# Performance work log

Hardware: AMD Instinct MI355X
Metric: run time of the kernel (lower is better)

The kernel has to match this reference:

```python
import jax, jax.numpy as jnp
import numpy as np

EPS = 1e-5

def _causal_conv(x, w):
    # x: [B, Cin, S], w: [Cout, Cin, K]; left-pad by K-1 for causality
    k = w.shape[-1]
    x = jnp.pad(x, ((0, 0), (0, 0), (k - 1, 0)))
    return jax.lax.conv_general_dilated(x, w, (1,), 'VALID',
                                        dimension_numbers=('NCH', 'OIH', 'NCH'))

def _activate_norm(x):
    # relu -> mean-center over last axis -> scaled L2 normalize over last axis
    x = jax.nn.relu(x)
    x = x - x.mean(-1, keepdims=True)
    n = x.shape[-1]
    denom = (jnp.sqrt(jnp.sum(x * x, axis=-1, keepdims=True)) + EPS) * (n ** -0.5)
    return x / denom

def _feed_forward(x, w0, w1, w2):
    x = _causal_conv(x, w0)
    x = _activate_norm(x)
    x = _causal_conv(x, w1)
    x = _activate_norm(x)
    return _causal_conv(x, w2)

def setup_inputs() -> dict:
    key = jax.random.key(0)
    B, F, S = 4, 1024, 2048
    I, K = 2048, 5
    ks = jax.random.split(key, 12)
    def w(k, shape):
        fan_in = shape[1] * shape[2]
        return jax.random.normal(k, shape, jnp.float32) * (fan_in ** -0.5)
    inp = jax.random.normal(ks[0], (B, F, S), jnp.float32)
    pos_embd = jax.random.normal(ks[1], (1, F, S), jnp.float32) * 0.02
    divisor = jax.random.uniform(ks[2], (1, F, S), jnp.float32) + 0.5  # bounded away from 0
    return {
        'inp': inp, 'pos_embd': pos_embd, 'divisor': divisor,
        'dw0': w(ks[3], (I, F, 1)), 'dw1': w(ks[4], (I, I, K)), 'dw2': w(ks[5], (F, I, 1)),
        'sw0': w(ks[6], (I, F, 1)), 'sw1': w(ks[7], (I, I, K)), 'sw2': w(ks[8], (F, I, 1)),
        'hw0': w(ks[9], (I, F, 1)), 'hw1': w(ks[10], (I, I, K)), 'hw2': w(ks[11], (F, I, 1)),
    }

def reference(inp, pos_embd, divisor, dw0, dw1, dw2, sw0, sw1, sw2, hw0, hw1, hw2):
    out = inp + pos_embd
    depth = _feed_forward(out, dw0, dw1, dw2)
    scale = _feed_forward(out, sw0, sw1, sw2)
    shift = _feed_forward(out, hw0, hw1, hw2)
    # linear attention: cumsum over dim 1 (as in source), divide, scale/shift, norm, residual
    return inp + _activate_norm(jnp.cumsum(depth, axis=1) / divisor * scale + shift)
```

## Files before the change

### kernel.cpp

```cpp
#include <hip/hip_runtime.h>
#include <math.h>

#define BSZ 4
#define FCH 1024
#define SEQ 2048
#define ICH 2048
#define KW  5
#define EPSV 1e-5f
#define RPAD 2244
#define NCHF 16

typedef __attribute__((ext_vector_type(8))) short bf16x8;
typedef __attribute__((ext_vector_type(4))) float f32x4;
typedef __attribute__((ext_vector_type(4))) unsigned short us4;

__device__ __forceinline__ unsigned short f2bf(float f) {
  union { float f; unsigned u; } v; v.f = f;
  unsigned r = v.u + 0x7fff + ((v.u >> 16) & 1);
  return (unsigned short)(r >> 16);
}
__device__ __forceinline__ float bf2f(unsigned short u) {
  union { unsigned u; float f; } v; v.u = (unsigned)u << 16; return v.f;
}

__device__ __forceinline__ void gload_lds16(const void* g, void* l) {
  __builtin_amdgcn_global_load_lds(
      (const __attribute__((address_space(1))) void*)g,
      (__attribute__((address_space(3))) void*)l, 16, 0, 0);
}

__global__ __launch_bounds__(256) void addpos_T_kernel(
    const float* __restrict__ inp, const float* __restrict__ pos,
    unsigned short* __restrict__ X)
{
  __shared__ float t[64][65];
  const int s0 = blockIdx.x * 64, f0 = blockIdx.y * 64, b = blockIdx.z;
  const int a = threadIdx.x & 63, g = threadIdx.x >> 6;
  const float* ib = inp + (size_t)b * FCH * SEQ;
#pragma unroll
  for (int i = 0; i < 16; ++i) {
    const size_t o = (size_t)(f0 + g + i * 4) * SEQ + s0 + a;
    t[a][g + i * 4] = ib[o] + pos[o];
  }
  __syncthreads();
#pragma unroll
  for (int i = 0; i < 16; ++i)
    X[(size_t)b * RPAD * FCH + (size_t)(4 + s0 + g + i * 4) * FCH + f0 + a] =
        f2bf(t[g + i * 4][a]);
}

__global__ __launch_bounds__(256) void zero_xpad_kernel(unsigned short* __restrict__ X)
{
  const int i = blockIdx.x * 256 + threadIdx.x;
  const int b = i / (4 * FCH);
  const int r = i % (4 * FCH);
  X[(size_t)b * RPAD * FCH + r] = 0;
}

__global__ __launch_bounds__(256) void transpose_div_kernel(
    const float* __restrict__ D, float* __restrict__ O)
{
  __shared__ float t[64][65];
  const int s0 = blockIdx.x * 64, f0 = blockIdx.y * 64;
  const int a = threadIdx.x & 63, g = threadIdx.x >> 6;
#pragma unroll
  for (int i = 0; i < 16; ++i)
    t[a][g + i * 4] = D[(size_t)(f0 + g + i * 4) * SEQ + s0 + a];
  __syncthreads();
#pragma unroll
  for (int i = 0; i < 16; ++i)
    O[(size_t)(s0 + g + i * 4) * FCH + f0 + a] = t[g + i * 4][a];
}

__global__ __launch_bounds__(256) void cast_bf_kernel(
    const float* __restrict__ I, unsigned short* __restrict__ O)
{
  const size_t i = ((size_t)blockIdx.x * 256 + threadIdx.x) * 4;
  const float4 v = *(const float4*)(I + i);
  us4 o; o.x = f2bf(v.x); o.y = f2bf(v.y); o.z = f2bf(v.z); o.w = f2bf(v.w);
  *(us4*)(O + i) = o;
}

__global__ __launch_bounds__(256) void cast_w1_kernel(
    const float* __restrict__ W, unsigned short* __restrict__ O)
{
  const int c = blockIdx.x * 256 + threadIdx.x;
  const int m = blockIdx.y;
  const float* s = W + ((size_t)m * ICH + c) * KW;
#pragma unroll
  for (int k = 0; k < KW; ++k)
    O[((size_t)k * ICH + m) * ICH + c] = f2bf(s[k]);
}

template <int BN, int NTAPS, int BF16OUT>
__global__ __launch_bounds__(512, 2) void gemm256_kernel(
    const unsigned short* __restrict__ A, const unsigned short* __restrict__ W,
    void* __restrict__ Cv, int M, int K,
    float* __restrict__ P1, float* __restrict__ P2)
{
  extern __shared__ __align__(16) char lds[];
  constexpr int ABYTES = 32768;
  constexpr int BBYTES = BN * 128;
  constexpr int BUF = ABYTES + BBYTES;
  constexpr int WN  = BN / 4;
  constexpr int JF  = BN / 64;
  constexpr int JF2 = BN / 128;

  const int tid = threadIdx.x;
  const int ln  = tid & 63;
  const int wv  = tid >> 6;
  const int wr  = wv >> 2;
  const int wc  = wv & 3;
  const int l15 = ln & 15;
  const int lhi = ln >> 4;

  const int s0 = blockIdx.x * 256;
  const int m0 = blockIdx.y * BN;
  const int b  = blockIdx.z;

  const char* Ab = (const char*)(A + (size_t)b * RPAD * K);
  const char* Wb = (const char*)W;
  const size_t MK = (size_t)M * K;
  const int KT = K >> 6;

  const int scs  = (((tid & 7) ^ ((tid >> 3) & 7)) << 4);
  const int rxor = (l15 & 7) << 4;
  const int cbx0 = (lhi * 16) ^ rxor;
  const int cbx1 = (lhi * 16 + 64) ^ rxor;

  f32x4 acc[8][JF] = {};

  auto STAGE = [&](int t, int k0, int pb) {
    const int roff = (NTAPS == 1) ? 4 : t;
    char* dst = lds + pb * BUF;
#pragma unroll
    for (int q = 0; q < 4; ++q) {
      const int row = (q * 512 + tid) >> 3;
      gload_lds16(Ab + (size_t)(s0 + row + roff) * ((size_t)K * 2) +
                      (size_t)(k0 * 2 + scs),
                  dst + q * 8192 + tid * 16);
    }
#pragma unroll
    for (int q = 0; q < BN / 64; ++q) {
      const int row = (q * 512 + tid) >> 3;
      gload_lds16(Wb + ((size_t)t * MK + (size_t)(m0 + row) * K + k0) * 2 + scs,
                  dst + ABYTES + q * 8192 + tid * 16);
    }
  };

  auto COMPUTE = [&](int pb) {
    const char* bb = lds + pb * BUF;
#pragma unroll
    for (int ih = 0; ih < 2; ++ih) {
      bf16x8 af[4][2];
#pragma unroll
      for (int i = 0; i < 4; ++i) {
        const int r = (wr * 128 + ih * 64 + i * 16 + l15) * 128;
        af[i][0] = *(const bf16x8*)(bb + r + cbx0);
        af[i][1] = *(const bf16x8*)(bb + r + cbx1);
      }
#pragma unroll
      for (int jh = 0; jh < 2; ++jh) {
        bf16x8 bfr[JF2][2];
#pragma unroll
        for (int j = 0; j < JF2; ++j) {
          const int r = ABYTES + (wc * WN + jh * (WN / 2) + j * 16 + l15) * 128;
          bfr[j][0] = *(const bf16x8*)(bb + r + cbx0);
          bfr[j][1] = *(const bf16x8*)(bb + r + cbx1);
        }
        __builtin_amdgcn_s_setprio(1);
#pragma unroll
        for (int i = 0; i < 4; ++i)
#pragma unroll
          for (int j = 0; j < JF2; ++j) {
            acc[ih * 4 + i][jh * JF2 + j] = __builtin_amdgcn_mfma_f32_16x16x32_bf16(
                af[i][0], bfr[j][0], acc[ih * 4 + i][jh * JF2 + j], 0, 0, 0);
            acc[ih * 4 + i][jh * JF2 + j] = __builtin_amdgcn_mfma_f32_16x16x32_bf16(
                af[i][1], bfr[j][1], acc[ih * 4 + i][jh * JF2 + j], 0, 0, 0);
          }
        __builtin_amdgcn_s_setprio(0);
      }
    }
  };

  STAGE(0, 0, 0);
  asm volatile("s_waitcnt vmcnt(0)" ::: "memory");
  __syncthreads();
  int p = 0;
  for (int t = 0; t < NTAPS; ++t) {
    for (int kt = 0; kt < KT; ++kt) {
      int ntp = t, nk = kt + 1;
      if (nk == KT) { nk = 0; ++ntp; }
      if (ntp < NTAPS) STAGE(ntp, nk * 64, p ^ 1);
      COMPUTE(p);
      asm volatile("s_waitcnt vmcnt(0)" ::: "memory");
      __syncthreads();
      p ^= 1;
    }
  }

  if constexpr (BF16OUT) {
    unsigned short* Cb = (unsigned short*)Cv + (size_t)b * SEQ * M;
    float S[JF] = {}, Q[JF] = {};
#pragma unroll
    for (int i = 0; i < 8; ++i) {
      const int sb = s0 + wr * 128 + i * 16 + lhi * 4;
#pragma unroll
      for (int j = 0; j < JF; ++j) {
        const int m = m0 + wc * WN + j * 16 + l15;
#pragma unroll
        for (int r = 0; r < 4; ++r) {
          const float x = fmaxf(acc[i][j][r], 0.f);
          S[j] += x; Q[j] += x * x;
          Cb[(size_t)(sb + r) * M + m] = f2bf(x);
        }
      }
    }
#pragma unroll
    for (int j = 0; j < JF; ++j) {
      S[j] += __shfl_xor(S[j], 16, 64); S[j] += __shfl_xor(S[j], 32, 64);
      Q[j] += __shfl_xor(Q[j], 16, 64); Q[j] += __shfl_xor(Q[j], 32, 64);
    }
    float* SL = (float*)lds;
    float* QL = SL + 2 * 4 * JF * 16;
    if (lhi == 0) {
#pragma unroll
      for (int j = 0; j < JF; ++j) {
        SL[((wr * 4 + wc) * JF + j) * 16 + l15] = S[j];
        QL[((wr * 4 + wc) * JF + j) * 16 + l15] = Q[j];
      }
    }
    __syncthreads();
    if (wr == 0 && lhi == 0) {
#pragma unroll
      for (int j = 0; j < JF; ++j) {
        const int m = m0 + wc * WN + j * 16 + l15;
        const size_t o = ((size_t)b * (SEQ / 256) + blockIdx.x) * M + m;
        P1[o] = SL[((0 * 4 + wc) * JF + j) * 16 + l15] +
                SL[((1 * 4 + wc) * JF + j) * 16 + l15];
        P2[o] = QL[((0 * 4 + wc) * JF + j) * 16 + l15] +
                QL[((1 * 4 + wc) * JF + j) * 16 + l15];
      }
    }
  } else {
    float* Cb = (float*)Cv + (size_t)b * SEQ * M;
#pragma unroll
    for (int i = 0; i < 8; ++i) {
      const int sb = s0 + wr * 128 + i * 16 + lhi * 4;
#pragma unroll
      for (int j = 0; j < JF; ++j) {
        const int m = m0 + wc * WN + j * 16 + l15;
#pragma unroll
        for (int r = 0; r < 4; ++r)
          Cb[(size_t)(sb + r) * M + m] = acc[i][j][r];
      }
    }
  }
}

__global__ __launch_bounds__(256) void colred_kernel(
    const float* __restrict__ Cf, float* __restrict__ P1,
    float* __restrict__ P2, int M)
{
  const int b = blockIdx.z;
  const int mi = threadIdx.x & 63;
  const int sg = threadIdx.x >> 6;
  const int m = blockIdx.x * 64 + mi;
  const int s0 = blockIdx.y * 128;
  const float* src = Cf + ((size_t)b * SEQ + s0) * M + m;
  float sum = 0.f, sq = 0.f;
  for (int s = sg; s < 128; s += 4) {
    const float x = fmaxf(src[(size_t)s * M], 0.f);
    sum += x; sq += x * x;
  }
  __shared__ float rs[4][64], rq[4][64];
  rs[sg][mi] = sum; rq[sg][mi] = sq;
  __syncthreads();
  if (sg == 0) {
    const size_t o = ((size_t)b * NCHF + blockIdx.y) * M + m;
    P1[o] = rs[0][mi] + rs[1][mi] + rs[2][mi] + rs[3][mi];
    P2[o] = rq[0][mi] + rq[1][mi] + rq[2][mi] + rq[3][mi];
  }
}

__global__ __launch_bounds__(256) void colfin_kernel(
    const float* __restrict__ P1, const float* __restrict__ P2,
    float* __restrict__ MS, int M, int nchunk)
{
  const int i = blockIdx.x * 256 + threadIdx.x;
  const int b = i / M, m = i % M;
  float S1 = 0.f, S2 = 0.f;
  for (int c = 0; c < nchunk; ++c) {
    S1 += P1[((size_t)b * nchunk + c) * M + m];
    S2 += P2[((size_t)b * nchunk + c) * M + m];
  }
  const float mean = S1 * (1.f / SEQ);
  const float ss = fmaxf(S2 - SEQ * mean * mean, 0.f);
  const float scl = sqrtf((float)SEQ) / (sqrtf(ss) + EPSV);
  MS[((size_t)b * 2 + 0) * M + m] = mean;
  MS[((size_t)b * 2 + 1) * M + m] = scl;
}

__global__ __launch_bounds__(256) void colapply_kernel(
    const unsigned short* __restrict__ Cf, const float* __restrict__ MS,
    unsigned short* __restrict__ Ob, int M)
{
  const int b = blockIdx.z;
  const int mi = threadIdx.x & 63;
  const int sg = threadIdx.x >> 6;
  const int m = blockIdx.x * 64 + mi;
  const int s0 = blockIdx.y * 128;
  const float mean = MS[((size_t)b * 2 + 0) * M + m];
  const float scl  = MS[((size_t)b * 2 + 1) * M + m];
  const unsigned short* src = Cf + ((size_t)b * SEQ + s0) * M + m;
  unsigned short* dst = Ob + ((size_t)b * RPAD + 4 + s0) * M + m;
  if (blockIdx.y == 0 && sg == 0) {
#pragma unroll
    for (int r = 0; r < 4; ++r) Ob[((size_t)b * RPAD + r) * M + m] = 0;
  }
  for (int s = sg; s < 128; s += 4)
    dst[(size_t)s * M] = f2bf((bf2f(src[(size_t)s * M]) - mean) * scl);
}

__global__ __launch_bounds__(256) void combine_kernel(
    float* __restrict__ Dp, const float* __restrict__ divT,
    const float* __restrict__ Sc, const float* __restrict__ Sh)
{
  const int row = blockIdx.x * 4 + (threadIdx.x >> 6);
  const int b = row >> 11, s = row & 2047;
  const int ln = threadIdx.x & 63;
  const size_t base = ((size_t)b * SEQ + s) * FCH;
  const float* dv = divT + (size_t)s * FCH;
  float carry = 0.f;
  for (int c0 = 0; c0 < FCH; c0 += 64) {
    float x = Dp[base + c0 + ln];
#pragma unroll
    for (int d = 1; d < 64; d <<= 1) {
      const float t = __shfl_up(x, d, 64);
      if (ln >= d) x += t;
    }
    x += carry;
    carry = __shfl(x, 63, 64);
    Dp[base + c0 + ln] = x / dv[c0 + ln] * Sc[base + c0 + ln] + Sh[base + c0 + ln];
  }
}

__global__ __launch_bounds__(256) void final_apply_kernel(
    const float* __restrict__ Df, const float* __restrict__ MS,
    const float* __restrict__ inp, float* __restrict__ out)
{
  __shared__ float tile[64][65];
  const int b = blockIdx.z;
  const int s0 = blockIdx.x * 64, f0 = blockIdx.y * 64;
  const int a = threadIdx.x & 63, g = threadIdx.x >> 6;
  const float mean = MS[((size_t)b * 2 + 0) * FCH + f0 + a];
  const float scl  = MS[((size_t)b * 2 + 1) * FCH + f0 + a];
#pragma unroll
  for (int i = 0; i < 16; ++i) {
    const int s = g + i * 4;
    const float x = fmaxf(Df[((size_t)b * SEQ + s0 + s) * FCH + f0 + a], 0.f);
    tile[s][a] = (x - mean) * scl;
  }
  __syncthreads();
#pragma unroll
  for (int i = 0; i < 16; ++i) {
    const int f = g + i * 4;
    const size_t o = ((size_t)b * FCH + f0 + f) * SEQ + s0 + a;
    out[o] = inp[o] + tile[a][f];
  }
}

extern "C" void kernel_launch(void* const* d_in, const int* in_sizes, int n_in,
                              void* d_out, int out_size, void* d_ws, size_t ws_size,
                              hipStream_t stream)
{
  const float* inp     = (const float*)d_in[0];
  const float* pos     = (const float*)d_in[1];
  const float* divisor = (const float*)d_in[2];
  const float* w_[9];
  for (int i = 0; i < 9; ++i) w_[i] = (const float*)d_in[3 + i];
  float* out = (float*)d_out;

  char* p = (char*)d_ws;
  float*          divT = (float*)p;          p += (size_t)SEQ * FCH * 4;
  unsigned short* Xbf  = (unsigned short*)p; p += (size_t)BSZ * RPAD * FCH * 2;
  unsigned short* T0b  = (unsigned short*)p; p += (size_t)BSZ * RPAD * ICH * 2;
  unsigned short* Cfb  = (unsigned short*)p; p += (size_t)BSZ * SEQ * ICH * 2;
  float*          Df   = (float*)p;          p += (size_t)BSZ * SEQ * FCH * 4;
  float*          Sf   = (float*)p;          p += (size_t)BSZ * SEQ * FCH * 4;
  float*          Hf   = (float*)p;          p += (size_t)BSZ * SEQ * FCH * 4;
  unsigned short* w0b  = (unsigned short*)p; p += (size_t)ICH * FCH * 2;
  unsigned short* w1b  = (unsigned short*)p; p += (size_t)KW * ICH * ICH * 2;
  unsigned short* w2b  = (unsigned short*)p; p += (size_t)FCH * ICH * 2;
  float*          P1   = (float*)p;          p += (size_t)BSZ * NCHF * ICH * 4;
  float*          P2   = (float*)p;          p += (size_t)BSZ * NCHF * ICH * 4;
  float*          MS   = (float*)p;          p += (size_t)BSZ * 2 * ICH * 4;

  hipFuncSetAttribute((const void*)gemm256_kernel<256, 1, 1>,
                      hipFuncAttributeMaxDynamicSharedMemorySize, 131072);
  hipFuncSetAttribute((const void*)gemm256_kernel<256, 5, 1>,
                      hipFuncAttributeMaxDynamicSharedMemorySize, 131072);
  hipFuncSetAttribute((const void*)gemm256_kernel<128, 1, 0>,
                      hipFuncAttributeMaxDynamicSharedMemorySize, 98304);

  zero_xpad_kernel<<<BSZ * 4 * FCH / 256, 256, 0, stream>>>(Xbf);
  addpos_T_kernel<<<dim3(SEQ / 64, FCH / 64, BSZ), 256, 0, stream>>>(inp, pos, Xbf);
  transpose_div_kernel<<<dim3(SEQ / 64, FCH / 64), 256, 0, stream>>>(divisor, divT);

  auto act_norm = [&](unsigned short* dst, int M) {
    colfin_kernel<<<(BSZ * M) / 256, 256, 0, stream>>>(P1, P2, MS, M, 8);
    colapply_kernel<<<dim3(M / 64, NCHF, BSZ), 256, 0, stream>>>(Cfb, MS, dst, M);
  };

  auto run_ff = [&](const float* w0, const float* w1, const float* w2, float* dst) {
    cast_bf_kernel<<<(ICH * FCH) / 1024, 256, 0, stream>>>(w0, w0b);
    cast_w1_kernel<<<dim3(ICH / 256, ICH), 256, 0, stream>>>(w1, w1b);
    cast_bf_kernel<<<(FCH * ICH) / 1024, 256, 0, stream>>>(w2, w2b);
    gemm256_kernel<256, 1, 1><<<dim3(SEQ / 256, ICH / 256, BSZ), 512, 131072, stream>>>(
        Xbf, w0b, Cfb, ICH, FCH, P1, P2);
    act_norm(T0b, ICH);
    gemm256_kernel<256, 5, 1><<<dim3(SEQ / 256, ICH / 256, BSZ), 512, 131072, stream>>>(
        T0b, w1b, Cfb, ICH, ICH, P1, P2);
    act_norm(T0b, ICH);
    gemm256_kernel<128, 1, 0><<<dim3(SEQ / 256, FCH / 128, BSZ), 512, 98304, stream>>>(
        T0b, w2b, dst, FCH, ICH, P1, P2);
  };

  run_ff(w_[0], w_[1], w_[2], Df);
  run_ff(w_[3], w_[4], w_[5], Sf);
  run_ff(w_[6], w_[7], w_[8], Hf);

  combine_kernel<<<(BSZ * SEQ) / 4, 256, 0, stream>>>(Df, divT, Sf, Hf);

  colred_kernel<<<dim3(FCH / 64, NCHF, BSZ), 256, 0, stream>>>(Df, P1, P2, FCH);
  colfin_kernel<<<(BSZ * FCH) / 256, 256, 0, stream>>>(P1, P2, MS, FCH, NCHF);
  final_apply_kernel<<<dim3(SEQ / 64, FCH / 64, BSZ), 256, 0, stream>>>(
      Df, MS, inp, out);
}
```

Measured before the change: 1.239 ms.

## Split tile loads into halves and interleave prefetch with phased MFMA compute

Restructures the GEMM main loop into a flattened tap/k iteration with four compute phases per tile. Global-to-LDS loads are split into two halves issued at different points, so half of the next-next tile is prefetched while the current tile computes. Partial vmcnt waits and raw s_barrier calls replace the full vmcnt(0) plus __syncthreads. This aims to overlap memory latency with MFMA work more finely, at the cost of more barriers per tile and subtler LDS buffer-reuse ordering. A sync is added before the epilogue reuses LDS.

```diff
diff --git a/kernel.cpp b/kernel.cpp
--- a/kernel.cpp
+++ b/kernel.cpp
@@ -104,7 +104,7 @@
   constexpr int BUF = ABYTES + BBYTES;
   constexpr int WN  = BN / 4;
   constexpr int JF  = BN / 64;
-  constexpr int JF2 = BN / 128;
+  constexpr int BH  = BN / 128;
 
   const int tid = threadIdx.x;
   const int ln  = tid & 63;
@@ -122,80 +122,81 @@
   const char* Wb = (const char*)W;
   const size_t MK = (size_t)M * K;
   const int KT = K >> 6;
-
-  const int scs  = (((tid & 7) ^ ((tid >> 3) & 7)) << 4);
-  const int rxor = (l15 & 7) << 4;
-  const int cbx0 = (lhi * 16) ^ rxor;
-  const int cbx1 = (lhi * 16 + 64) ^ rxor;
+  const int T  = NTAPS * KT;
+
+  const int scs = (((tid & 7) ^ ((tid >> 3) & 7)) << 4);
 
   f32x4 acc[8][JF] = {};
 
-  auto STAGE = [&](int t, int k0, int pb) {
+  auto ISSUE = [&](int tau, int h) {
+    const int t  = tau / KT;
+    const int k0 = (tau - t * KT) * 64;
     const int roff = (NTAPS == 1) ? 4 : t;
-    char* dst = lds + pb * BUF;
-#pragma unroll
-    for (int q = 0; q < 4; ++q) {
-      const int row = (q * 512 + tid) >> 3;
+    char* dst = lds + (tau & 1) * BUF;
+#pragma unroll
+    for (int q = 0; q < 2; ++q) {
+      const int row = h * 128 + q * 64 + (tid >> 3);
       gload_lds16(Ab + (size_t)(s0 + row + roff) * ((size_t)K * 2) +
                       (size_t)(k0 * 2 + scs),
-                  dst + q * 8192 + tid * 16);
-    }
-#pragma unroll
-    for (int q = 0; q < BN / 64; ++q) {
-      const int row = (q * 512 + tid) >> 3;
-      gload_lds16(Wb + ((size_t)t * MK + (size_t)(m0 + row) * K + k0) * 2 + scs,
-                  dst + ABYTES + q * 8192 + tid * 16);
+                  dst + h * 16384 + q * 8192 + tid * 16);
+    }
+    if (h == 0 || BH == 2) {
+#pragma unroll
+      for (int q = 0; q < 2; ++q) {
+        const int row = h * 128 + q * 64 + (tid >> 3);
+        gload_lds16(Wb + ((size_t)t * MK + (size_t)(m0 + row) * K + k0) * 2 + scs,
+                    dst + ABYTES + h * 16384 + q * 8192 + tid * 16);
+      }
     }
   };
 
-  auto COMPUTE = [&](int pb) {
-    const char* bb = lds + pb * BUF;
-#pragma unroll
-    for (int ih = 0; ih < 2; ++ih) {
-      bf16x8 af[4][2];
+  ISSUE(0, 0); ISSUE(0, 1);
+  if (T > 1) {
+    ISSUE(1, 0);
+    asm volatile("s_waitcnt vmcnt(4)" ::: "memory");
+  } else {
+    asm volatile("s_waitcnt vmcnt(0)" ::: "memory");
+  }
+  __builtin_amdgcn_s_barrier();
+
+  for (int tau = 0; tau < T; ++tau) {
+    const char* bb = lds + (tau & 1) * BUF;
+#pragma unroll
+    for (int ph = 0; ph < 4; ++ph) {
+      const int ih = ph >> 1, ks = ph & 1;
+      bf16x8 af[4], bw[JF];
 #pragma unroll
       for (int i = 0; i < 4; ++i) {
-        const int r = (wr * 128 + ih * 64 + i * 16 + l15) * 128;
-        af[i][0] = *(const bf16x8*)(bb + r + cbx0);
-        af[i][1] = *(const bf16x8*)(bb + r + cbx1);
-      }
-#pragma unroll
-      for (int jh = 0; jh < 2; ++jh) {
-        bf16x8 bfr[JF2][2];
-#pragma unroll
-        for (int j = 0; j < JF2; ++j) {
-          const int r = ABYTES + (wc * WN + jh * (WN / 2) + j * 16 + l15) * 128;
-          bfr[j][0] = *(const bf16x8*)(bb + r + cbx0);
-          bfr[j][1] = *(const bf16x8*)(bb + r + cbx1);
-        }
-        __builtin_amdgcn_s_setprio(1);
-#pragma unroll
-        for (int i = 0; i < 4; ++i)
-#pragma unroll
-          for (int j = 0; j < JF2; ++j) {
-            acc[ih * 4 + i][jh * JF2 + j] = __builtin_amdgcn_mfma_f32_16x16x32_bf16(
-                af[i][0], bfr[j][0], acc[ih * 4 + i][jh * JF2 + j], 0, 0, 0);
-            acc[ih * 4 + i][jh * JF2 + j] = __builtin_amdgcn_mfma_f32_16x16x32_bf16(
-                af[i][1], bfr[j][1], acc[ih * 4 + i][jh * JF2 + j], 0, 0, 0);
-          }
-        __builtin_amdgcn_s_setprio(0);
-      }
-    }
-  };
-
-  STAGE(0, 0, 0);
-  asm volatile("s_waitcnt vmcnt(0)" ::: "memory");
-  __syncthreads();
-  int p = 0;
-  for (int t = 0; t < NTAPS; ++t) {
-    for (int kt = 0; kt < KT; ++kt) {
-      int ntp = t, nk = kt + 1;
-      if (nk == KT) { nk = 0; ++ntp; }
-      if (ntp < NTAPS) STAGE(ntp, nk * 64, p ^ 1);
-      COMPUTE(p);
+        const int r = wr * 128 + ih * 64 + i * 16 + l15;
+        af[i] = *(const bf16x8*)(bb + r * 128 +
+                                 ((lhi * 16 + ks * 64) ^ ((r & 7) << 4)));
+      }
+#pragma unroll
+      for (int j = 0; j < JF; ++j) {
+        const int r = wc * WN + j * 16 + l15;
+        bw[j] = *(const bf16x8*)(bb + ABYTES + r * 128 +
+                                 ((lhi * 16 + ks * 64) ^ ((r & 7) << 4)));
+      }
+      if (ph == 0 && tau + 1 < T) ISSUE(tau + 1, 1);
+      __builtin_amdgcn_s_barrier();
+      asm volatile("s_waitcnt lgkmcnt(0)" ::: "memory");
+      __builtin_amdgcn_s_setprio(1);
+#pragma unroll
+      for (int i = 0; i < 4; ++i)
+#pragma unroll
+        for (int j = 0; j < JF; ++j)
+          acc[ih * 4 + i][j] = __builtin_amdgcn_mfma_f32_16x16x32_bf16(
+              af[i], bw[j], acc[ih * 4 + i][j], 0, 0, 0);
+      __builtin_amdgcn_s_setprio(0);
+      __builtin_amdgcn_s_barrier();
+    }
+    if (tau + 2 < T) {
+      ISSUE(tau + 2, 0);
+      asm volatile("s_waitcnt vmcnt(4)" ::: "memory");
+      __builtin_amdgcn_s_barrier();
+    } else if (tau + 1 < T) {
       asm volatile("s_waitcnt vmcnt(0)" ::: "memory");
-      __syncthreads();
-      p ^= 1;
+      __builtin_amdgcn_s_barrier();
     }
   }
 
@@ -223,6 +224,7 @@
     }
     float* SL = (float*)lds;
     float* QL = SL + 2 * 4 * JF * 16;
+    __syncthreads();
     if (lhi == 0) {
 #pragma unroll
       for (int j = 0; j < JF; ++j) {
```

After: 1.409 ms. 13.7% more time.
